# Kernel optimization log

Hardware: AMD Instinct MI355X
Metric: run time of the kernel (lower is better)

Reference implementation:

```python
import jax, jax.numpy as jnp
import numpy as np

B, T, F, H = 32768, 64, 8, 16
NUM_LABELS, OUT_WIN = 4, 8
FC1_OUT = F * T          # 512
FC2_OUT = NUM_LABELS * OUT_WIN  # 32


def _lstm_relu(x_tbf, W, U, b):
    """Keras LSTM with activation='relu', recurrent_activation='sigmoid'.
    x_tbf: [T, B, F_in]. Returns all hidden states [T, B, H].
    Gate order in Keras kernel: i, f, c, o."""
    Bv = x_tbf.shape[1]
    h0 = jnp.zeros((Bv, H), x_tbf.dtype)
    c0 = jnp.zeros((Bv, H), x_tbf.dtype)

    def step(carry, xt):
        h, c = carry
        z = xt @ W + h @ U + b  # [B, 4H]
        i, f, g, o = jnp.split(z, 4, axis=-1)
        i = jax.nn.sigmoid(i)
        f = jax.nn.sigmoid(f)
        o = jax.nn.sigmoid(o)
        c = f * c + i * jax.nn.relu(g)
        h = o * jax.nn.relu(c)
        return (h, c), h

    _, hs = jax.lax.scan(step, (h0, c0), x_tbf)
    return hs  # [T, B, H]


def setup_inputs() -> dict:
    key = jax.random.key(0)
    ks = jax.random.split(key, 12)
    s = lambda fan_in: 1.0 / np.sqrt(fan_in)
    x = jax.random.normal(ks[0], (B, T, F), dtype=jnp.float32)
    W1 = jax.random.normal(ks[1], (F, 4 * H), dtype=jnp.float32) * s(F)
    U1 = jax.random.normal(ks[2], (H, 4 * H), dtype=jnp.float32) * s(H)
    b1 = jnp.zeros((4 * H,), jnp.float32)
    W2 = jax.random.normal(ks[3], (H, 4 * H), dtype=jnp.float32) * s(H)
    U2 = jax.random.normal(ks[4], (H, 4 * H), dtype=jnp.float32) * s(H)
    b2 = jnp.zeros((4 * H,), jnp.float32)
    Wfc1 = jax.random.normal(ks[5], (H, FC1_OUT), dtype=jnp.float32) * s(H)
    bfc1 = jnp.zeros((FC1_OUT,), jnp.float32)
    Wfc2 = jax.random.normal(ks[6], (FC1_OUT, FC2_OUT), dtype=jnp.float32) * s(FC1_OUT)
    bfc2 = jnp.zeros((FC2_OUT,), jnp.float32)
    return {"x": x, "W1": W1, "U1": U1, "b1": b1, "W2": W2, "U2": U2,
            "b2": b2, "Wfc1": Wfc1, "bfc1": bfc1, "Wfc2": Wfc2, "bfc2": bfc2}


def reference(x, W1, U1, b1, W2, U2, b2, Wfc1, bfc1, Wfc2, bfc2):
    x_tbf = jnp.transpose(x, (1, 0, 2))        # [T, B, F]
    h1 = _lstm_relu(x_tbf, W1, U1, b1)         # [T, B, H] (return_sequences=True)
    h2 = _lstm_relu(h1, W2, U2, b2)[-1]        # [B, H] (return_sequences=False)
    # Dropout is identity at inference (training=False).
    y = jax.nn.relu(h2 @ Wfc1 + bfc1)          # [B, 512]
    y = y @ Wfc2 + bfc2                        # [B, 32]
    return y
```

## Files before the change

### kernel.cpp

```cpp
#include <hip/hip_runtime.h>
#include <stdint.h>


#define NT 64
#define NF 8

typedef __attribute__((ext_vector_type(8))) short bf16x8;
typedef __attribute__((ext_vector_type(4))) float f32x4;
typedef __attribute__((ext_vector_type(2))) unsigned int u32x2;
typedef __attribute__((ext_vector_type(4))) unsigned int u32x4;

#define MFMA16 __builtin_amdgcn_mfma_f32_16x16x32_bf16

static __device__ __forceinline__ uint32_t cvt_pk(float a, float b) {
  uint32_t r;
  asm("v_cvt_pk_bf16_f32 %0, %1, %2" : "=v"(r) : "v"(a), "v"(b));
  return r;
}
static __device__ __forceinline__ void pack_hl(float a, float b,
                                               uint32_t& hi, uint32_t& lo) {
  hi = cvt_pk(a, b);
  float ha = __uint_as_float(hi << 16);
  float hb = __uint_as_float(hi & 0xFFFF0000u);
  lo = cvt_pk(a - ha, b - hb);
}
static __device__ __forceinline__ void split_hl(float f, short& hi, short& lo) {
  uint32_t w = cvt_pk(f, 0.f);
  hi = (short)(w & 0xFFFFu);
  float hf = __uint_as_float(w << 16);
  uint32_t wl = cvt_pk(f - hf, 0.f);
  lo = (short)(wl & 0xFFFFu);
}
static __device__ __forceinline__ float sigmoidf_(float v) {
  return __builtin_amdgcn_rcpf(1.0f + __expf(-v));
}
static __device__ __forceinline__ bf16x8 asbf(u32x4 w) {
  union { u32x4 u; bf16x8 b; } c; c.u = w; return c.b;
}
static __device__ __forceinline__ uint32_t bperm(int addr, uint32_t v) {
  return (uint32_t)__builtin_amdgcn_ds_bpermute(addr, (int)v);
}
static __device__ __forceinline__ void lds_fence() {
  asm volatile("s_waitcnt lgkmcnt(0)" ::: "memory");
}

__global__ __launch_bounds__(256, 2) void lstm_fused(
    const float* __restrict__ x,
    const float* __restrict__ W1, const float* __restrict__ U1, const float* __restrict__ b1,
    const float* __restrict__ W2, const float* __restrict__ U2, const float* __restrict__ b2,
    const float* __restrict__ Wfc1, const float* __restrict__ bfc1,
    const float* __restrict__ Wfc2, const float* __restrict__ bfc2,
    float* __restrict__ out)
{
  const int tid  = threadIdx.x;
  const int lane = tid & 63;
  const int wv   = tid >> 6;
  const int col  = lane & 15;
  const int g    = lane >> 4;
  const int base = (blockIdx.x * 4 + wv) * 16;

  __shared__ __align__(16) char cf[4][2][16 * 80];
  char* const cfh = &cf[wv][0][0];
  char* const cfl = &cf[wv][1][0];

  bf16x8 B1a[4], B2a[4], B1b[4], B2b[4];
#pragma unroll
  for (int n = 0; n < 4; ++n) {
    const int c = 16 * n + col;
#pragma unroll
    for (int j = 0; j < 8; ++j) {
      const int k = 8 * g + j;
      short h, l;
      if (k < 8)       { split_hl(W1[k * 64 + c], h, l);        B1a[n][j] = h; B2a[n][j] = l; }
      else if (k < 16) { split_hl(W1[(k - 8) * 64 + c], h, l);  B1a[n][j] = h; B2a[n][j] = 0; }
      else             { split_hl(U1[(k - 16) * 64 + c], h, l); B1a[n][j] = h; B2a[n][j] = l; }
      short h2, l2;
      if (k < 16) split_hl(W2[k * 64 + c], h2, l2);
      else        split_hl(U2[(k - 16) * 64 + c], h2, l2);
      B1b[n][j] = h2; B2b[n][j] = l2;
    }
  }

  f32x4 bias1v[4], bias2v[4];
#pragma unroll
  for (int n = 0; n < 4; ++n) {
    bias1v[n] = *(const f32x4*)(b1 + 16 * n + 4 * g);
    bias2v[n] = *(const f32x4*)(b2 + 16 * n + 4 * g);
  }

  const int addrA = ((g & 1) * 32 + col) * 4;
  const int addrB = addrA + 64;

  f32x4 c1 = {0.f, 0.f, 0.f, 0.f};
  f32x4 c2 = {0.f, 0.f, 0.f, 0.f};
  uint32_t h1ph[4] = {0,0,0,0}, h1pl[4] = {0,0,0,0};
  uint32_t h2ph[4] = {0,0,0,0}, h2pl[4] = {0,0,0,0};

  const float* xrow = x + (size_t)(base + col) * (NT * NF);
  f32x4 xa = *(const f32x4*)(xrow);
  f32x4 xb = *(const f32x4*)(xrow + 4);

  for (int i = 0; i < NT; ++i) {
    u32x4 l2b1w, l2b3w;
#pragma unroll
    for (int q = 0; q < 4; ++q) {
      l2b1w[q] = (g < 2) ? h1ph[q] : h2ph[q];
      l2b3w[q] = (g < 2) ? h1pl[q] : h2pl[q];
    }
    uint32_t xh[4], xl[4];
    pack_hl(xa[0], xa[1], xh[0], xl[0]);
    pack_hl(xa[2], xa[3], xh[1], xl[1]);
    pack_hl(xb[0], xb[1], xh[2], xl[2]);
    pack_hl(xb[2], xb[3], xh[3], xl[3]);
    if (i + 1 < NT) {
      xa = *(const f32x4*)(xrow + (i + 1) * NF);
      xb = *(const f32x4*)(xrow + (i + 1) * NF + 4);
    }
    u32x4 l1b1w, l1b3w;
#pragma unroll
    for (int q = 0; q < 4; ++q) {
      uint32_t xw = (g == 0) ? xh[q] : xl[q];
      l1b1w[q] = (g < 2) ? xw : h1ph[q];
      l1b3w[q] = (g < 2) ? 0u : h1pl[q];
    }
    bf16x8 L1B1 = asbf(l1b1w), L1B3 = asbf(l1b3w);
    bf16x8 L2B1 = asbf(l2b1w), L2B3 = asbf(l2b3w);

    f32x4 z[4], y[4];
#pragma unroll
    for (int n = 0; n < 4; ++n) {
      f32x4 zi = MFMA16(B1a[n], L1B1, bias1v[n], 0, 0, 0);
      zi = MFMA16(B2a[n], L1B1, zi, 0, 0, 0);
      zi = MFMA16(B1a[n], L1B3, zi, 0, 0, 0);
      z[n] = zi;
      f32x4 yi = MFMA16(B1b[n], L2B1, bias2v[n], 0, 0, 0);
      yi = MFMA16(B2b[n], L2B1, yi, 0, 0, 0);
      yi = MFMA16(B1b[n], L2B3, yi, 0, 0, 0);
      y[n] = yi;
    }

    f32x4 h1v;
#pragma unroll
    for (int r = 0; r < 4; ++r) {
      float ig = sigmoidf_(z[0][r]);
      float fg = sigmoidf_(z[1][r]);
      float gg = fmaxf(z[2][r], 0.f);
      float og = sigmoidf_(z[3][r]);
      float cc = fg * c1[r] + ig * gg;
      c1[r] = cc;
      h1v[r] = og * fmaxf(cc, 0.f);
    }
    {
      uint32_t p01h, p01l, p23h, p23l;
      pack_hl(h1v[0], h1v[1], p01h, p01l);
      pack_hl(h1v[2], h1v[3], p23h, p23l);
      h1ph[0] = bperm(addrA, p01h); h1ph[1] = bperm(addrA, p23h);
      h1ph[2] = bperm(addrB, p01h); h1ph[3] = bperm(addrB, p23h);
      h1pl[0] = bperm(addrA, p01l); h1pl[1] = bperm(addrA, p23l);
      h1pl[2] = bperm(addrB, p01l); h1pl[3] = bperm(addrB, p23l);
    }

    f32x4 h2v;
    if (i != 0) {
#pragma unroll
      for (int r = 0; r < 4; ++r) {
        float ig = sigmoidf_(y[0][r]);
        float fg = sigmoidf_(y[1][r]);
        float gg = fmaxf(y[2][r], 0.f);
        float og = sigmoidf_(y[3][r]);
        float cc = fg * c2[r] + ig * gg;
        c2[r] = cc;
        h2v[r] = og * fmaxf(cc, 0.f);
      }
    } else {
      h2v = (f32x4){0.f, 0.f, 0.f, 0.f};
    }
    {
      uint32_t p01h, p01l, p23h, p23l;
      pack_hl(h2v[0], h2v[1], p01h, p01l);
      pack_hl(h2v[2], h2v[3], p23h, p23l);
      h2ph[0] = bperm(addrA, p01h); h2ph[1] = bperm(addrA, p23h);
      h2ph[2] = bperm(addrB, p01h); h2ph[3] = bperm(addrB, p23h);
      h2pl[0] = bperm(addrA, p01l); h2pl[1] = bperm(addrA, p23l);
      h2pl[2] = bperm(addrB, p01l); h2pl[3] = bperm(addrB, p23l);
    }
  }

  {
    u32x4 b1w, b3w;
#pragma unroll
    for (int q = 0; q < 4; ++q) {
      b1w[q] = (g < 2) ? h1ph[q] : h2ph[q];
      b3w[q] = (g < 2) ? h1pl[q] : h2pl[q];
    }
    bf16x8 L2B1 = asbf(b1w), L2B3 = asbf(b3w);
    f32x4 y[4];
#pragma unroll
    for (int n = 0; n < 4; ++n) {
      f32x4 yi = MFMA16(B1b[n], L2B1, bias2v[n], 0, 0, 0);
      yi = MFMA16(B2b[n], L2B1, yi, 0, 0, 0);
      yi = MFMA16(B1b[n], L2B3, yi, 0, 0, 0);
      y[n] = yi;
    }
    f32x4 h2v;
#pragma unroll
    for (int r = 0; r < 4; ++r) {
      float ig = sigmoidf_(y[0][r]);
      float fg = sigmoidf_(y[1][r]);
      float gg = fmaxf(y[2][r], 0.f);
      float og = sigmoidf_(y[3][r]);
      float cc = fg * c2[r] + ig * gg;
      c2[r] = cc;
      h2v[r] = og * fmaxf(cc, 0.f);
    }
    uint32_t p01h, p01l, p23h, p23l;
    pack_hl(h2v[0], h2v[1], p01h, p01l);
    pack_hl(h2v[2], h2v[3], p23h, p23l);
    h2ph[0] = bperm(addrA, p01h); h2ph[1] = bperm(addrA, p23h);
    h2ph[2] = bperm(addrB, p01h); h2ph[3] = bperm(addrB, p23h);
    h2pl[0] = bperm(addrA, p01l); h2pl[1] = bperm(addrA, p23l);
    h2pl[2] = bperm(addrB, p01l); h2pl[3] = bperm(addrB, p23l);
  }

  u32x4 bwf;
#pragma unroll
  for (int q = 0; q < 4; ++q) bwf[q] = (g < 2) ? h2ph[q] : h2pl[q];
  bf16x8 Bfc = asbf(bwf);

  f32x4 acc2[2];
#pragma unroll
  for (int nn = 0; nn < 2; ++nn)
    acc2[nn] = *(const f32x4*)(bfc2 + 16 * nn + 4 * g);

  for (int kc = 0; kc < 16; ++kc) {
#pragma unroll
    for (int t = 0; t < 2; ++t) {
      const int mt = 2 * kc + t;
      bf16x8 A1h, A1l;
#pragma unroll
      for (int j = 0; j < 8; ++j) {
        float w = Wfc1[((8 * g + j) & 15) * 512 + 16 * mt + col];
        short h, l; split_hl(w, h, l);
        A1h[j] = h; A1l[j] = l;
      }
      f32x4 bv = *(const f32x4*)(bfc1 + 16 * mt + 4 * g);
      f32x4 acc = MFMA16(A1h, Bfc, bv, 0, 0, 0);
      acc = MFMA16(A1l, Bfc, acc, 0, 0, 0);
      uint32_t q01h, q01l, q23h, q23l;
      pack_hl(fmaxf(acc[0], 0.f), fmaxf(acc[1], 0.f), q01h, q01l);
      pack_hl(fmaxf(acc[2], 0.f), fmaxf(acc[3], 0.f), q23h, q23l);
      *(u32x2*)(cfh + col * 80 + 32 * t + 8 * g) = (u32x2){q01h, q23h};
      *(u32x2*)(cfl + col * 80 + 32 * t + 8 * g) = (u32x2){q01l, q23l};
    }
    lds_fence();
    bf16x8 Bh = *(const bf16x8*)(cfh + col * 80 + 16 * g);
    bf16x8 Bl = *(const bf16x8*)(cfl + col * 80 + 16 * g);
#pragma unroll
    for (int nn = 0; nn < 2; ++nn) {
      bf16x8 A2h, A2l;
#pragma unroll
      for (int j = 0; j < 8; ++j) {
        float w = Wfc2[(size_t)(32 * kc + 8 * g + j) * 32 + 16 * nn + col];
        short h, l; split_hl(w, h, l);
        A2h[j] = h; A2l[j] = l;
      }
      acc2[nn] = MFMA16(A2h, Bh, acc2[nn], 0, 0, 0);
      acc2[nn] = MFMA16(A2h, Bl, acc2[nn], 0, 0, 0);
      acc2[nn] = MFMA16(A2l, Bh, acc2[nn], 0, 0, 0);
    }
    lds_fence();
  }

#pragma unroll
  for (int nn = 0; nn < 2; ++nn)
    *(f32x4*)(out + (size_t)(base + col) * 32 + 16 * nn + 4 * g) = acc2[nn];
}

extern "C" void kernel_launch(void* const* d_in, const int* in_sizes, int n_in,
                              void* d_out, int out_size, void* d_ws, size_t ws_size,
                              hipStream_t stream) {
  const float* x    = (const float*)d_in[0];
  const float* W1   = (const float*)d_in[1];
  const float* U1   = (const float*)d_in[2];
  const float* b1   = (const float*)d_in[3];
  const float* W2   = (const float*)d_in[4];
  const float* U2   = (const float*)d_in[5];
  const float* b2   = (const float*)d_in[6];
  const float* Wfc1 = (const float*)d_in[7];
  const float* bfc1 = (const float*)d_in[8];
  const float* Wfc2 = (const float*)d_in[9];
  const float* bfc2 = (const float*)d_in[10];

  lstm_fused<<<dim3(512), dim3(256), 0, stream>>>(
      x, W1, U1, b1, W2, U2, b2, Wfc1, bfc1, Wfc2, bfc2, (float*)d_out);
}
```

Measured before the change: 219.8 us.

## Replace ds_bpermute hidden-state exchange with v_permlane32_swap and permuted K mapping

```diff
diff --git a/kernel.cpp b/kernel.cpp
--- a/kernel.cpp
+++ b/kernel.cpp
@@ -37,11 +37,14 @@
 static __device__ __forceinline__ bf16x8 asbf(u32x4 w) {
   union { u32x4 u; bf16x8 b; } c; c.u = w; return c.b;
 }
-static __device__ __forceinline__ uint32_t bperm(int addr, uint32_t v) {
-  return (uint32_t)__builtin_amdgcn_ds_bpermute(addr, (int)v);
+static __device__ __forceinline__ void pl32(uint32_t& a, uint32_t& b) {
+  asm("v_permlane32_swap_b32 %0, %1" : "+v"(a), "+v"(b));
 }
 static __device__ __forceinline__ void lds_fence() {
   asm volatile("s_waitcnt lgkmcnt(0)" ::: "memory");
+}
+static __device__ __forceinline__ int unitmap(int g, int j) {
+  return 4 * (g & 1) + (j & 3) + 8 * (j >> 2);
 }
 
 __global__ __launch_bounds__(256, 2) void lstm_fused(
@@ -69,14 +72,14 @@
     const int c = 16 * n + col;
 #pragma unroll
     for (int j = 0; j < 8; ++j) {
-      const int k = 8 * g + j;
+      const int u = unitmap(g, j);
       short h, l;
-      if (k < 8)       { split_hl(W1[k * 64 + c], h, l);        B1a[n][j] = h; B2a[n][j] = l; }
-      else if (k < 16) { split_hl(W1[(k - 8) * 64 + c], h, l);  B1a[n][j] = h; B2a[n][j] = 0; }
-      else             { split_hl(U1[(k - 16) * 64 + c], h, l); B1a[n][j] = h; B2a[n][j] = l; }
+      if (g == 0)      { split_hl(W1[j * 64 + c], h, l); B1a[n][j] = h; B2a[n][j] = l; }
+      else if (g == 1) { split_hl(W1[j * 64 + c], h, l); B1a[n][j] = h; B2a[n][j] = 0; }
+      else             { split_hl(U1[u * 64 + c], h, l); B1a[n][j] = h; B2a[n][j] = l; }
       short h2, l2;
-      if (k < 16) split_hl(W2[k * 64 + c], h2, l2);
-      else        split_hl(U2[(k - 16) * 64 + c], h2, l2);
+      if (g < 2) split_hl(W2[u * 64 + c], h2, l2);
+      else       split_hl(U2[u * 64 + c], h2, l2);
       B1b[n][j] = h2; B2b[n][j] = l2;
     }
   }
@@ -88,25 +91,16 @@
     bias2v[n] = *(const f32x4*)(b2 + 16 * n + 4 * g);
   }
 
-  const int addrA = ((g & 1) * 32 + col) * 4;
-  const int addrB = addrA + 64;
-
   f32x4 c1 = {0.f, 0.f, 0.f, 0.f};
   f32x4 c2 = {0.f, 0.f, 0.f, 0.f};
-  uint32_t h1ph[4] = {0,0,0,0}, h1pl[4] = {0,0,0,0};
-  uint32_t h2ph[4] = {0,0,0,0}, h2pl[4] = {0,0,0,0};
+  uint32_t h1p[4] = {0, 0, 0, 0};
+  uint32_t h2p[4] = {0, 0, 0, 0};
 
   const float* xrow = x + (size_t)(base + col) * (NT * NF);
   f32x4 xa = *(const f32x4*)(xrow);
   f32x4 xb = *(const f32x4*)(xrow + 4);
 
   for (int i = 0; i < NT; ++i) {
-    u32x4 l2b1w, l2b3w;
-#pragma unroll
-    for (int q = 0; q < 4; ++q) {
-      l2b1w[q] = (g < 2) ? h1ph[q] : h2ph[q];
-      l2b3w[q] = (g < 2) ? h1pl[q] : h2pl[q];
-    }
     uint32_t xh[4], xl[4];
     pack_hl(xa[0], xa[1], xh[0], xl[0]);
     pack_hl(xa[2], xa[3], xh[1], xl[1]);
@@ -116,15 +110,24 @@
       xa = *(const f32x4*)(xrow + (i + 1) * NF);
       xb = *(const f32x4*)(xrow + (i + 1) * NF + 4);
     }
-    u32x4 l1b1w, l1b3w;
-#pragma unroll
-    for (int q = 0; q < 4; ++q) {
-      uint32_t xw = (g == 0) ? xh[q] : xl[q];
-      l1b1w[q] = (g < 2) ? xw : h1ph[q];
-      l1b3w[q] = (g < 2) ? 0u : h1pl[q];
-    }
-    bf16x8 L1B1 = asbf(l1b1w), L1B3 = asbf(l1b3w);
-    bf16x8 L2B1 = asbf(l2b1w), L2B3 = asbf(l2b3w);
+
+    uint32_t S0 = (g & 1) ? xl[0] : xh[0];
+    { uint32_t t = (g & 1) ? xl[2] : xh[2]; S0 = (g & 2) ? t : S0; }
+    uint32_t S1 = (g & 1) ? xl[1] : xh[1];
+    { uint32_t t = (g & 1) ? xl[3] : xh[3]; S1 = (g & 2) ? t : S1; }
+    uint32_t a0 = S0, a2 = h1p[0]; pl32(a0, a2);
+    uint32_t a1 = S1, a3 = h1p[1]; pl32(a1, a3);
+    uint32_t e0 = 0,  e2 = h1p[2]; pl32(e0, e2);
+    uint32_t e1 = 0,  e3 = h1p[3]; pl32(e1, e3);
+    bf16x8 L1B1 = asbf((u32x4){a0, a1, a2, a3});
+    bf16x8 L1B3 = asbf((u32x4){e0, e1, e2, e3});
+
+    uint32_t m0 = h1p[0], m2 = h2p[0]; pl32(m0, m2);
+    uint32_t m1 = h1p[1], m3 = h2p[1]; pl32(m1, m3);
+    uint32_t n0 = h1p[2], n2 = h2p[2]; pl32(n0, n2);
+    uint32_t n1 = h1p[3], n3 = h2p[3]; pl32(n1, n3);
+    bf16x8 L2B1 = asbf((u32x4){m0, m1, m2, m3});
+    bf16x8 L2B3 = asbf((u32x4){n0, n1, n2, n3});
 
     f32x4 z[4], y[4];
 #pragma unroll
@@ -132,10 +135,12 @@
       f32x4 zi = MFMA16(B1a[n], L1B1, bias1v[n], 0, 0, 0);
       zi = MFMA16(B2a[n], L1B1, zi, 0, 0, 0);
       zi = MFMA16(B1a[n], L1B3, zi, 0, 0, 0);
+      asm("" : "+v"(zi));
       z[n] = zi;
       f32x4 yi = MFMA16(B1b[n], L2B1, bias2v[n], 0, 0, 0);
       yi = MFMA16(B2b[n], L2B1, yi, 0, 0, 0);
       yi = MFMA16(B1b[n], L2B3, yi, 0, 0, 0);
+      asm("" : "+v"(yi));
       y[n] = yi;
     }
 
@@ -150,15 +155,8 @@
       c1[r] = cc;
       h1v[r] = og * fmaxf(cc, 0.f);
     }
-    {
-      uint32_t p01h, p01l, p23h, p23l;
-      pack_hl(h1v[0], h1v[1], p01h, p01l);
-      pack_hl(h1v[2], h1v[3], p23h, p23l);
-      h1ph[0] = bperm(addrA, p01h); h1ph[1] = bperm(addrA, p23h);
-      h1ph[2] = bperm(addrB, p01h); h1ph[3] = bperm(addrB, p23h);
-      h1pl[0] = bperm(addrA, p01l); h1pl[1] = bperm(addrA, p23l);
-      h1pl[2] = bperm(addrB, p01l); h1pl[3] = bperm(addrB, p23l);
-    }
+    pack_hl(h1v[0], h1v[1], h1p[0], h1p[2]);
+    pack_hl(h1v[2], h1v[3], h1p[1], h1p[3]);
 
     f32x4 h2v;
     if (i != 0) {
@@ -175,25 +173,17 @@
     } else {
       h2v = (f32x4){0.f, 0.f, 0.f, 0.f};
     }
-    {
-      uint32_t p01h, p01l, p23h, p23l;
-      pack_hl(h2v[0], h2v[1], p01h, p01l);
-      pack_hl(h2v[2], h2v[3], p23h, p23l);
-      h2ph[0] = bperm(addrA, p01h); h2ph[1] = bperm(addrA, p23h);
-      h2ph[2] = bperm(addrB, p01h); h2ph[3] = bperm(addrB, p23h);
-      h2pl[0] = bperm(addrA, p01l); h2pl[1] = bperm(addrA, p23l);
-      h2pl[2] = bperm(addrB, p01l); h2pl[3] = bperm(addrB, p23l);
-    }
+    pack_hl(h2v[0], h2v[1], h2p[0], h2p[2]);
+    pack_hl(h2v[2], h2v[3], h2p[1], h2p[3]);
   }
 
   {
-    u32x4 b1w, b3w;
-#pragma unroll
-    for (int q = 0; q < 4; ++q) {
-      b1w[q] = (g < 2) ? h1ph[q] : h2ph[q];
-      b3w[q] = (g < 2) ? h1pl[q] : h2pl[q];
-    }
-    bf16x8 L2B1 = asbf(b1w), L2B3 = asbf(b3w);
+    uint32_t m0 = h1p[0], m2 = h2p[0]; pl32(m0, m2);
+    uint32_t m1 = h1p[1], m3 = h2p[1]; pl32(m1, m3);
+    uint32_t n0 = h1p[2], n2 = h2p[2]; pl32(n0, n2);
+    uint32_t n1 = h1p[3], n3 = h2p[3]; pl32(n1, n3);
+    bf16x8 L2B1 = asbf((u32x4){m0, m1, m2, m3});
+    bf16x8 L2B3 = asbf((u32x4){n0, n1, n2, n3});
     f32x4 y[4];
 #pragma unroll
     for (int n = 0; n < 4; ++n) {
@@ -213,19 +203,13 @@
       c2[r] = cc;
       h2v[r] = og * fmaxf(cc, 0.f);
     }
-    uint32_t p01h, p01l, p23h, p23l;
-    pack_hl(h2v[0], h2v[1], p01h, p01l);
-    pack_hl(h2v[2], h2v[3], p23h, p23l);
-    h2ph[0] = bperm(addrA, p01h); h2ph[1] = bperm(addrA, p23h);
-    h2ph[2] = bperm(addrB, p01h); h2ph[3] = bperm(addrB, p23h);
-    h2pl[0] = bperm(addrA, p01l); h2pl[1] = bperm(addrA, p23l);
-    h2pl[2] = bperm(addrB, p01l); h2pl[3] = bperm(addrB, p23l);
-  }
-
-  u32x4 bwf;
-#pragma unroll
-  for (int q = 0; q < 4; ++q) bwf[q] = (g < 2) ? h2ph[q] : h2pl[q];
-  bf16x8 Bfc = asbf(bwf);
+    pack_hl(h2v[0], h2v[1], h2p[0], h2p[2]);
+    pack_hl(h2v[2], h2v[3], h2p[1], h2p[3]);
+  }
+
+  uint32_t f0 = h2p[0], f2 = h2p[2]; pl32(f0, f2);
+  uint32_t f1 = h2p[1], f3 = h2p[3]; pl32(f1, f3);
+  bf16x8 Bfc = asbf((u32x4){f0, f1, f2, f3});
 
   f32x4 acc2[2];
 #pragma unroll
@@ -239,7 +223,7 @@
       bf16x8 A1h, A1l;
 #pragma unroll
       for (int j = 0; j < 8; ++j) {
-        float w = Wfc1[((8 * g + j) & 15) * 512 + 16 * mt + col];
+        float w = Wfc1[unitmap(g, j) * 512 + 16 * mt + col];
         short h, l; split_hl(w, h, l);
         A1h[j] = h; A1l[j] = l;
       }
```

Result: no change. 220.8 us (+0.4%).
